# Optimization experiments

Measured on AMD Instinct MI355X. Metric: run time of the kernel, lower is better.

The kernel has to match this reference:

```python
import jax, jax.numpy as jnp
import numpy as np
from jax import lax

PRE_NMS_TOP_N = 2000
POST_NMS_TOP_N = 1000
NMS_THRESH = 0.7
MIN_SIZE = 0.0
BBOX_XFORM_CLIP = float(np.log(1000.0 / 16.0))
NEG = jnp.float32(-1e30)


def setup_inputs() -> dict:
    key = jax.random.key(0)
    k1, k2, k3, k4, k5 = jax.random.split(key, 5)
    N, A, H, W = 16, 3, 256, 336
    img_h, img_w = 1024, 1344
    num = A * H * W  # 258048 anchors per image
    objectness = jax.random.normal(k1, (N, A, H, W), jnp.float32)
    box_regression = jax.random.normal(k2, (N, A * 4, H, W), jnp.float32) * 0.5
    # synthetic but valid xyxy anchors (x2 > x1, y2 > y1)
    cx = jax.random.uniform(k3, (N, num)) * img_w
    cy = jax.random.uniform(k4, (N, num)) * img_h
    wh = 16.0 + jax.random.uniform(k5, (N, num, 2)) * 256.0
    anchors = jnp.stack([cx - 0.5 * wh[..., 0], cy - 0.5 * wh[..., 1],
                         cx + 0.5 * wh[..., 0], cy + 0.5 * wh[..., 1]], axis=-1)
    return {"anchors": anchors.astype(jnp.float32), "objectness": objectness,
            "box_regression": box_regression, "img_h": img_h, "img_w": img_w}


def box_decode(codes, anchors):
    # BoxCoder(weights=(1,1,1,1)).decode, TO_REMOVE=1 convention
    w = anchors[..., 2] - anchors[..., 0] + 1.0
    h = anchors[..., 3] - anchors[..., 1] + 1.0
    ctr_x = anchors[..., 0] + 0.5 * w
    ctr_y = anchors[..., 1] + 0.5 * h
    dx, dy, dw, dh = codes[..., 0], codes[..., 1], codes[..., 2], codes[..., 3]
    dw = jnp.minimum(dw, BBOX_XFORM_CLIP)
    dh = jnp.minimum(dh, BBOX_XFORM_CLIP)
    pcx = dx * w + ctr_x
    pcy = dy * h + ctr_y
    pw = jnp.exp(dw) * w
    ph = jnp.exp(dh) * h
    return jnp.stack([pcx - 0.5 * pw, pcy - 0.5 * ph,
                      pcx + 0.5 * pw - 1.0, pcy + 0.5 * ph - 1.0], axis=-1)


def pairwise_iou(boxes):
    area = (boxes[:, 2] - boxes[:, 0] + 1.0) * (boxes[:, 3] - boxes[:, 1] + 1.0)
    lt = jnp.maximum(boxes[:, None, :2], boxes[None, :, :2])  # [K,K,2]
    rb = jnp.minimum(boxes[:, None, 2:], boxes[None, :, 2:])
    wh = jnp.maximum(rb - lt + 1.0, 0.0)
    inter = wh[..., 0] * wh[..., 1]
    return inter / (area[:, None] + area[None, :] - inter)


def nms_keep(boxes, valid):
    # boxes already sorted by score desc; greedy suppression scan over rows
    K = boxes.shape[0]
    iou = pairwise_iou(boxes)  # [K,K]
    idx = jnp.arange(K)

    def body(keep, xs):
        row, i = xs
        sup = keep[i] & (idx > i) & (row > NMS_THRESH)
        return keep & ~sup, None

    keep, _ = lax.scan(body, valid, (iou, idx))
    return keep


def reference(anchors, objectness, box_regression, img_h, img_w):
    N, A, H, W = objectness.shape
    # permute_and_flatten: (N,A,H,W) -> (N, H*W*A)
    obj = jax.nn.sigmoid(jnp.transpose(objectness, (0, 2, 3, 1)).reshape(N, -1))
    breg = jnp.transpose(box_regression.reshape(N, A, 4, H, W), (0, 3, 4, 1, 2)).reshape(N, -1, 4)
    k = min(PRE_NMS_TOP_N, obj.shape[1])
    scores, topk_idx = lax.top_k(obj, k)  # sorted desc
    batch = jnp.arange(N)[:, None]
    breg = breg[batch, topk_idx]        # [N,k,4]
    anc = anchors[batch, topk_idx]      # [N,k,4]
    boxes = box_decode(breg, anc)       # [N,k,4]
    # clip_to_image (TO_REMOVE=1)
    x1 = jnp.clip(boxes[..., 0], 0.0, img_w - 1)
    y1 = jnp.clip(boxes[..., 1], 0.0, img_h - 1)
    x2 = jnp.clip(boxes[..., 2], 0.0, img_w - 1)
    y2 = jnp.clip(boxes[..., 3], 0.0, img_h - 1)
    boxes = jnp.stack([x1, y1, x2, y2], axis=-1)
    # remove_small_boxes as a validity mask (fixed shape)
    ws = x2 - x1 + 1.0
    hs = y2 - y1 + 1.0
    valid = (ws >= MIN_SIZE) & (hs >= MIN_SIZE)
    keep = jax.vmap(nms_keep)(boxes, valid)  # [N,k]
    masked = jnp.where(keep, scores, NEG)
    final_scores, sel = lax.top_k(masked, POST_NMS_TOP_N)  # preserves score order
    final_boxes = boxes[batch, sel]
    # [N, post_nms_top_n, 5]: xyxy + objectness (padded slots have score ~ -1e30)
    return jnp.concatenate([final_boxes, final_scores[..., None]], axis=-1)
```

## Files before the change

kernel.cpp:

```cpp
#include <hip/hip_runtime.h>
#include <stdint.h>

#define NIMG 16
#define AANCH 3
#define HH 256
#define WW 336
#define HWP (HH*WW)
#define NUM (AANCH*HWP)
#define TOTAL (NIMG*NUM)
#define PRE_K 2000
#define POST_K 1000
#define NMS_TH 0.7f
#define NEGV -1e30f
#define CAND_CAP 4096
#define ROWS 2048
#define RWORDS 64
#define CHUNK 4096
#define CBLOCKS (NUM / CHUNK)
#define HPARTS 16
#define HBINS 4096
#define HCHUNK (NUM / HPARTS)

#define WS_HIST 0u
#define WS_COLT 0u
#define WS_CBOX 262144u
#define WS_CSCO 1310720u
#define WS_CUT  4194304u
#define WS_CNT  4194560u
#define WS_CAND 4194816u
#define WS_BOX  4719104u
#define WS_SCO  5243392u
#define WS_RMI  5374464u
#define WS_MASK 5444096u

__device__ __forceinline__ uint32_t fkey(float f){
    uint32_t b = __float_as_uint(f);
    return (b & 0x80000000u) ? ~b : (b | 0x80000000u);
}
__device__ __forceinline__ float keyf(uint32_t k){
    uint32_t b = (k & 0x80000000u) ? (k & 0x7FFFFFFFu) : ~k;
    return __uint_as_float(b);
}

__global__ __launch_bounds__(1024) void k_hist(const float* __restrict__ obj,
                                               uint32_t* __restrict__ part,
                                               uint32_t* __restrict__ cnt,
                                               uint32_t* __restrict__ rminit){
    int img = blockIdx.x >> 4;
    int blk = blockIdx.x & 15;
    int tid = threadIdx.x;
    if (blockIdx.x == 0){
        for (int i = tid; i < 32 + NIMG * RWORDS; i += 1024){
            if (i < 32) cnt[i] = 0u;
            else        rminit[i - 32] = 0u;
        }
    }
    __shared__ uint32_t h[HBINS];
    #pragma unroll
    for (int i = 0; i < HBINS / 1024; ++i) h[tid + i * 1024] = 0u;
    __syncthreads();
    const float* base = obj + (size_t)img * NUM + (size_t)blk * HCHUNK;
    for (int e = tid * 4; e < HCHUNK; e += 4096){
        float4 v = *(const float4*)(base + e);
        atomicAdd(&h[fkey(v.x) >> 20], 1u);
        atomicAdd(&h[fkey(v.y) >> 20], 1u);
        atomicAdd(&h[fkey(v.z) >> 20], 1u);
        atomicAdd(&h[fkey(v.w) >> 20], 1u);
    }
    __syncthreads();
    uint32_t* p = part + ((size_t)blockIdx.x) * HBINS;
    #pragma unroll
    for (int i = 0; i < HBINS / 1024; ++i) p[tid + i * 1024] = h[tid + i * 1024];
}

__global__ __launch_bounds__(1024) void k_binsel(const uint32_t* __restrict__ part,
                                                 uint32_t* __restrict__ cut,
                                                 uint32_t* __restrict__ nAout){
    int img = blockIdx.x, tid = threadIdx.x;
    const uint32_t* pb = part + (size_t)img * HPARTS * HBINS;
    int bin0 = HBINS - 4 * (tid + 1);
    uint32_t c0 = 0, c1 = 0, c2 = 0, c3 = 0;
    for (int k = 0; k < HPARTS; ++k){
        const uint4 v = *(const uint4*)(pb + (size_t)k * HBINS + bin0);
        c0 += v.x; c1 += v.y; c2 += v.z; c3 += v.w;
    }
    uint32_t s = c0 + c1 + c2 + c3;
    __shared__ uint32_t ss[1024];
    uint32_t x = s;
    ss[tid] = x; __syncthreads();
    for (int d = 1; d < 1024; d <<= 1){
        uint32_t y = (tid >= d) ? ss[tid - d] : 0u;
        __syncthreads();
        x += y; ss[tid] = x;
        __syncthreads();
    }
    uint32_t incl = x, excl = x - s;
    if (excl < PRE_K && incl >= PRE_K){
        uint32_t c = excl;
        uint32_t cc[4] = {c0, c1, c2, c3};
        for (int j = 3; j >= 0; --j){
            uint32_t cb = c;
            c += cc[j];
            if (c >= PRE_K){
                cut[img] = ((uint32_t)(bin0 + j)) << 20;
                nAout[img] = cb;
                break;
            }
        }
    }
}

__device__ __forceinline__ void emit_candidate(
        uint32_t key, uint32_t f, uint32_t pos, int img,
        const float* __restrict__ anchors, const float* __restrict__ breg,
        float imw, float imh,
        unsigned long long* __restrict__ cand,
        float4* __restrict__ cboxes, float* __restrict__ cscores){
    const float CLIPV = 4.135166556742356f;
    cand[img * CAND_CAP + pos] = ((unsigned long long)key << 32)
        | ((unsigned long long)((~f) & 0x3FFFFu) << 14) | (unsigned long long)pos;
    float logit = keyf(key);
    float sc = 1.0f / (1.0f + expf(-logit));
    const float* an = anchors + ((size_t)img * NUM + f) * 4;
    float ax1 = an[0], ay1 = an[1], ax2 = an[2], ay2 = an[3];
    int a = (int)(f % AANCH); int hw = (int)(f / AANCH);
    size_t bbase = ((size_t)img * 12 + a * 4) * HWP + (size_t)hw;
    float dx = breg[bbase], dy = breg[bbase + HWP];
    float dw = breg[bbase + 2 * (size_t)HWP], dh = breg[bbase + 3 * (size_t)HWP];
    float aw = ax2 - ax1 + 1.0f, ah = ay2 - ay1 + 1.0f;
    float cx = ax1 + 0.5f * aw, cy = ay1 + 0.5f * ah;
    dw = fminf(dw, CLIPV); dh = fminf(dh, CLIPV);
    float pcx = dx * aw + cx, pcy = dy * ah + cy;
    float pw = expf(dw) * aw, ph = expf(dh) * ah;
    float x1 = pcx - 0.5f * pw, y1 = pcy - 0.5f * ph;
    float x2 = pcx + 0.5f * pw - 1.0f, y2 = pcy + 0.5f * ph - 1.0f;
    x1 = fminf(fmaxf(x1, 0.0f), imw - 1.0f);
    y1 = fminf(fmaxf(y1, 0.0f), imh - 1.0f);
    x2 = fminf(fmaxf(x2, 0.0f), imw - 1.0f);
    y2 = fminf(fmaxf(y2, 0.0f), imh - 1.0f);
    bool valid = ((x2 - x1 + 1.0f) >= 0.0f) && ((y2 - y1 + 1.0f) >= 0.0f);
    cboxes[img * CAND_CAP + pos] = make_float4(x1, y1, x2, y2);
    cscores[img * CAND_CAP + pos] = valid ? sc : -sc;
}

__global__ __launch_bounds__(256) void k_compact(const float* __restrict__ obj,
                                                 const uint32_t* __restrict__ cut,
                                                 const uint32_t* __restrict__ nAarr,
                                                 uint32_t* __restrict__ cnt,
                                                 unsigned long long* __restrict__ cand,
                                                 const float* __restrict__ anchors,
                                                 const float* __restrict__ breg,
                                                 const int* __restrict__ pimh,
                                                 const int* __restrict__ pimw,
                                                 float4* __restrict__ cboxes,
                                                 float* __restrict__ cscores){
    int img   = blockIdx.x / CBLOCKS;
    int chunk = blockIdx.x - img * CBLOCKS;
    int base  = img * NUM + chunk * CHUNK;
    __shared__ uint32_t lcA, lcB, gbA, gbB;
    __shared__ uint2 lbuf[CHUNK];
    if (threadIdx.x == 0){ lcA = 0u; lcB = 0u; }
    __syncthreads();
    uint32_t cutv = cut[img];
    uint32_t cutbin = cutv >> 20;
    float4 v[4];
    #pragma unroll
    for (int it = 0; it < 4; ++it)
        v[it] = *(const float4*)(obj + base + it * 1024 + (int)threadIdx.x * 4);
    #pragma unroll
    for (int it = 0; it < 4; ++it){
        int e = it * 1024 + (int)threadIdx.x * 4;
        float vv[4] = {v[it].x, v[it].y, v[it].z, v[it].w};
        #pragma unroll
        for (int q = 0; q < 4; ++q){
            uint32_t k = fkey(vv[q]);
            if (k >= cutv){
                int r = chunk * CHUNK + e + q;
                int a = r / HWP, hw = r - a * HWP;
                uint32_t f = (uint32_t)(hw * AANCH + a);
                if ((k >> 20) > cutbin){
                    uint32_t p = atomicAdd(&lcA, 1u);
                    lbuf[p] = make_uint2(k, f);
                } else {
                    uint32_t p = atomicAdd(&lcB, 1u);
                    lbuf[CHUNK - 1 - p] = make_uint2(k, f);
                }
            }
        }
    }
    __syncthreads();
    if (threadIdx.x == 0){
        gbA = (lcA > 0u) ? atomicAdd(&cnt[img], lcA) : 0u;
        gbB = (lcB > 0u) ? atomicAdd(&cnt[16 + img], lcB) : 0u;
    }
    __syncthreads();
    uint32_t nA  = nAarr[img];
    uint32_t nAp = (nA + 1u) & ~1u;
    float imw = (float)(*pimw), imh = (float)(*pimh);
    uint32_t na = lcA, ga = gbA, nb = lcB, gb = gbB;
    for (uint32_t t = threadIdx.x; t < na; t += 256u){
        uint32_t pos = ga + t;
        uint2 kf = lbuf[t];
        emit_candidate(kf.x, kf.y, pos, img, anchors, breg, imw, imh,
                       cand, cboxes, cscores);
    }
    for (uint32_t t = threadIdx.x; t < nb; t += 256u){
        uint32_t pos = nAp + gb + t;
        if (pos < CAND_CAP){
            uint2 kf = lbuf[CHUNK - 1 - t];
            emit_candidate(kf.x, kf.y, pos, img, anchors, breg, imw, imh,
                           cand, cboxes, cscores);
        }
    }
}

__global__ __launch_bounds__(256) void k_rank(
        const unsigned long long* __restrict__ cand, const uint32_t* __restrict__ cnt,
        const uint32_t* __restrict__ nAarr,
        const float4* __restrict__ cboxes, const float* __restrict__ cscores,
        float4* __restrict__ boxes_s, float* __restrict__ scores_s,
        uint32_t* __restrict__ rminit){
    int img = blockIdx.x >> 4;
    int b   = blockIdx.x & 15;
    int tid = threadIdx.x;
    int e   = b * 256 + tid;
    uint32_t nA   = nAarr[img];
    uint32_t nAp  = (nA + 1u) & ~1u;
    uint32_t nB   = min(cnt[16 + img], (uint32_t)CAND_CAP - nAp);
    uint32_t end  = nAp + nB;
    uint32_t endp = (end + 1u) & ~1u;
    const unsigned long long* cp = cand + img * CAND_CAP;
    __shared__ alignas(16) unsigned long long tile[CAND_CAP];
    for (int i = tid; i < (int)endp; i += 256){
        bool v = (i < (int)nA) || (i >= (int)nAp && i < (int)end);
        tile[i] = v ? cp[i] : 0ull;
    }
    __syncthreads();
    bool inA = e < (int)nA;
    bool inB = (e >= (int)nAp) && (e < (int)end);
    bool validE = inA || inB;
    unsigned long long mine = validE ? tile[e] : ~0ull;
    int s0 = inA ? 0 : (inB ? (int)(nAp >> 1) : 0);
    int s1 = inA ? (int)(nAp >> 1) : (inB ? (int)(endp >> 1) : 0);
    int rank = inB ? (int)nA : 0;
    const ulonglong2* tile2 = (const ulonglong2*)tile;
    #pragma unroll 8
    for (int i = s0; i < s1; ++i){
        ulonglong2 p = tile2[i];
        rank += (p.x > mine) ? 1 : 0;
        rank += (p.y > mine) ? 1 : 0;
    }
    if (validE && rank < PRE_K){
        float4 bx = cboxes[img * CAND_CAP + e];
        float s   = cscores[img * CAND_CAP + e];
        boxes_s[img * ROWS + rank] = bx;
        scores_s[img * ROWS + rank] = fabsf(s);
        if (s < 0.0f) atomicOr(&rminit[img * RWORDS + (rank >> 5)], 1u << (rank & 31));
    }
}

__global__ __launch_bounds__(1024) void k_mask(const float4* __restrict__ boxes_s,
                                               uint32_t* __restrict__ mask,
                                               unsigned long long* __restrict__ colT){
    int img = blockIdx.x >> 4;
    int rc  = blockIdx.x & 15;
    int tid = threadIdx.x;
    int lane = tid & 63;
    int wv = tid >> 6;
    int gw = rc * 16 + wv;
    __shared__ float4 B[ROWS];
    __shared__ float  AR[ROWS];
    const float4* bp = boxes_s + img * ROWS;
    for (int t = tid; t < ROWS; t += 1024){
        float4 b = bp[t]; B[t] = b;
        AR[t] = (b.z - b.x + 1.0f) * (b.w - b.y + 1.0f);
    }
    __syncthreads();
    if (gw < 32){
        int j = lane;
        float4 bj = B[gw * 64 + j]; float aj = AR[gw * 64 + j];
        unsigned long long col = 0ull;
        #pragma unroll 8
        for (int i = 0; i < 64; ++i){
            float4 bi = B[gw * 64 + i]; float ai = AR[gw * 64 + i];
            float xx1 = fmaxf(bi.x, bj.x), yy1 = fmaxf(bi.y, bj.y);
            float xx2 = fminf(bi.z, bj.z), yy2 = fminf(bi.w, bj.w);
            float iw = fmaxf(xx2 - xx1 + 1.0f, 0.0f);
            float ih = fmaxf(yy2 - yy1 + 1.0f, 0.0f);
            float inter = iw * ih;
            bool pred = (i < j) && (inter > NMS_TH * (ai + aj - inter));
            col |= pred ? (1ull << i) : 0ull;
        }
        colT[(size_t)(img * 32 + gw) * 64 + j] = col;
    }
    uint32_t* M = mask + (size_t)img * ROWS * RWORDS;
    for (int i = gw; i < PRE_K; i += 256){
        float4 bi = B[i];
        float ai = AR[i];
        unsigned long long* Mrow = (unsigned long long*)(M + (size_t)i * RWORDS);
        for (int jb = (i >> 6); jb < 32; ++jb){
            int j = (jb << 6) + lane;
            bool pred = false;
            if (j > i && j < PRE_K){
                float4 bj = B[j];
                float xx1 = fmaxf(bi.x, bj.x), yy1 = fmaxf(bi.y, bj.y);
                float xx2 = fminf(bi.z, bj.z), yy2 = fminf(bi.w, bj.w);
                float iw = fmaxf(xx2 - xx1 + 1.0f, 0.0f);
                float ih = fmaxf(yy2 - yy1 + 1.0f, 0.0f);
                float inter = iw * ih;
                pred = inter > NMS_TH * (ai + AR[j] - inter);
            }
            unsigned long long bm = __ballot(pred);
            if (lane == 0) Mrow[jb] = bm;
        }
    }
}

__global__ __launch_bounds__(256) void k_scan(const uint32_t* __restrict__ mask,
                                              const unsigned long long* __restrict__ colT,
                                              const uint32_t* __restrict__ rminit,
                                              const float4* __restrict__ boxes_s,
                                              const float* __restrict__ scores_s,
                                              float* __restrict__ out){
    int img = blockIdx.x;
    int tid = threadIdx.x;
    int lane = tid & 63;
    int wv = tid >> 6;
    const uint32_t* M = mask + (size_t)img * ROWS * RWORDS;
    const unsigned long long* CT = colT + (size_t)img * 32 * 64;
    __shared__ uint32_t S[POST_K];
    __shared__ uint32_t acc_lds[4][64];
    __shared__ unsigned long long keep_lds;

    uint32_t rm = 0u;
    if (wv == 0){
        rm = rminit[img * RWORDS + lane];
        if (lane == 62) rm |= 0xFFFF0000u;
        if (lane == 63) rm  = 0xFFFFFFFFu;
    }
    unsigned long long colA = 0ull, colB = 0ull, rmb_sav = 0ull;
    uint32_t rowsA[16], rowsB[16];

#define PRELOAD(B, ROWSX)                                                       \
    {                                                                           \
        const uint32_t* Mb = M + (size_t)((B) * 64 + wv * 16) * RWORDS + lane;  \
        _Pragma("unroll")                                                       \
        for (int r = 0; r < 16; ++r) ROWSX[r] = Mb[(size_t)r * RWORDS];         \
    }
#define FIXED_POINT(B, COLX)                                                    \
    {                                                                           \
        uint32_t lo = __shfl(rm, 2 * (B)), hi = __shfl(rm, 2 * (B) + 1);        \
        unsigned long long inc = ((unsigned long long)hi << 32)                 \
                               | (unsigned long long)lo;                        \
        bool alivej = ((inc >> lane) & 1ull) == 0ull;                           \
        unsigned long long keep = ~inc;                                         \
        for (int it = 0; it < 66; ++it){                                        \
            bool ok = alivej && ((COLX & keep) == 0ull);                        \
            unsigned long long nk = __ballot(ok);                              \
            if (nk == keep) break;                                              \
            keep = nk;                                                          \
        }                                                                       \
        if (lane == 0) keep_lds = keep;                                         \
        rmb_sav = ~keep;                                                        \
    }
#define APPLY(ROWSX)                                                            \
    {                                                                           \
        unsigned long long kp = keep_lds;                                       \
        uint32_t acc = 0u;                                                      \
        _Pragma("unroll")                                                       \
        for (int r = 0; r < 16; ++r)                                            \
            acc |= ((kp >> (wv * 16 + r)) & 1ull) ? ROWSX[r] : 0u;              \
        acc_lds[wv][lane] = acc;                                                \
    }
#define FINISH(B)                                                               \
    {                                                                           \
        uint32_t acc = acc_lds[0][lane] | acc_lds[1][lane]                      \
                     | acc_lds[2][lane] | acc_lds[3][lane];                     \
        rm |= (lane >= 2 * (B)) ? acc : 0u;                                     \
        if (lane == 2 * (B))     rm = (uint32_t)rmb_sav;                        \
        if (lane == 2 * (B) + 1) rm = (uint32_t)(rmb_sav >> 32);                \
    }

    PRELOAD(0, rowsA);
    if (wv == 0) colA = CT[lane];

    #pragma unroll 1
    for (int b = 0; b < 32; b += 2){
        PRELOAD(b + 1, rowsB);
        if (wv == 0){
            colB = CT[(size_t)(b + 1) * 64 + lane];
            FIXED_POINT(b, colA);
        }
        __syncthreads();
        APPLY(rowsA);
        __syncthreads();
        if (wv == 0) FINISH(b);
        if (b + 2 < 32){
            PRELOAD(b + 2, rowsA);
            if (wv == 0) colA = CT[(size_t)(b + 2) * 64 + lane];
        }
        if (wv == 0) FIXED_POINT(b + 1, colB);
        __syncthreads();
        APPLY(rowsB);
        __syncthreads();
        if (wv == 0) FINISH(b + 1);
    }
#undef PRELOAD
#undef FIXED_POINT
#undef APPLY
#undef FINISH

    if (wv == 0){
        uint32_t inr = (lane < 62) ? 0xFFFFFFFFu : (lane == 62 ? 0x0000FFFFu : 0u);
        uint32_t kw = (~rm) & inr;
        uint32_t sw = rm & inr;
        uint32_t kc = __popc(kw);
        uint32_t x = kc;
        for (int d = 1; d < 64; d <<= 1){ uint32_t y = __shfl_up(x, d); if (lane >= d) x += y; }
        uint32_t kexcl = x - kc;
        uint32_t ktot = __shfl(x, 63);
        uint32_t m = kw; uint32_t r = 0;
        while (m){
            int bb = __ffs(m) - 1;
            uint32_t slot = kexcl + r;
            if (slot < POST_K) S[slot] = (uint32_t)(lane * 32 + bb) | 0x80000000u;
            m &= m - 1; ++r;
        }
        if (ktot < POST_K){
            uint32_t sc2 = __popc(sw);
            uint32_t x2 = sc2;
            for (int d = 1; d < 64; d <<= 1){ uint32_t y = __shfl_up(x2, d); if (lane >= d) x2 += y; }
            uint32_t sexcl = x2 - sc2;
            uint32_t m2 = sw; uint32_t r2 = 0;
            while (m2){
                int bb = __ffs(m2) - 1;
                uint32_t slot = ktot + sexcl + r2;
                if (slot >= ktot && slot < POST_K) S[slot] = (uint32_t)(lane * 32 + bb);
                m2 &= m2 - 1; ++r2;
            }
        }
    }
    __syncthreads();
    const float4* bp = boxes_s + img * ROWS;
    const float* sp = scores_s + img * ROWS;
    float* o = out + (size_t)img * POST_K * 5;
    for (int s = tid; s < POST_K; s += 256){
        uint32_t v = S[s];
        uint32_t pos = v & 0x7FFFFFFFu;
        bool kept = (v >> 31) != 0;
        float4 bx = bp[pos];
        float sc = kept ? sp[pos] : NEGV;
        float* oo = o + s * 5;
        oo[0] = bx.x; oo[1] = bx.y; oo[2] = bx.z; oo[3] = bx.w; oo[4] = sc;
    }
}

extern "C" void kernel_launch(void* const* d_in, const int* in_sizes, int n_in,
                              void* d_out, int out_size, void* d_ws, size_t ws_size,
                              hipStream_t stream) {
    const float* anchors = (const float*)d_in[0];
    const float* obj     = (const float*)d_in[1];
    const float* breg    = (const float*)d_in[2];
    const int*   pimh    = (const int*)d_in[3];
    const int*   pimw    = (const int*)d_in[4];
    float* out = (float*)d_out;
    uint8_t* ws = (uint8_t*)d_ws;

    uint32_t*           part     = (uint32_t*)(ws + WS_HIST);
    unsigned long long* colT     = (unsigned long long*)(ws + WS_COLT);
    float4*             cboxes   = (float4*)(ws + WS_CBOX);
    float*              cscores  = (float*)(ws + WS_CSCO);
    uint32_t*           cut      = (uint32_t*)(ws + WS_CUT);
    uint32_t*           nAarr    = (uint32_t*)(ws + WS_CUT + 64);
    uint32_t*           cnt      = (uint32_t*)(ws + WS_CNT);
    unsigned long long* cand     = (unsigned long long*)(ws + WS_CAND);
    float4*             boxes_s  = (float4*)(ws + WS_BOX);
    float*              scores_s = (float*)(ws + WS_SCO);
    uint32_t*           rminit   = (uint32_t*)(ws + WS_RMI);
    uint32_t*           mask     = (uint32_t*)(ws + WS_MASK);

    k_hist<<<NIMG * HPARTS, 1024, 0, stream>>>(obj, part, cnt, rminit);
    k_binsel<<<NIMG, 1024, 0, stream>>>(part, cut, nAarr);
    k_compact<<<NIMG * CBLOCKS, 256, 0, stream>>>(obj, cut, nAarr, cnt, cand,
                                                  anchors, breg, pimh, pimw,
                                                  cboxes, cscores);
    k_rank<<<NIMG * 16, 256, 0, stream>>>(cand, cnt, nAarr, cboxes, cscores,
                                          boxes_s, scores_s, rminit);
    k_mask<<<NIMG * 16, 1024, 0, stream>>>(boxes_s, mask, colT);
    k_scan<<<NIMG, 256, 0, stream>>>(mask, colT, rminit, boxes_s, scores_s, out);
}
```

Before: 138.8 us.

## Restructure NMS mask kernel so each lane computes a whole row word

The IoU mask kernel now maps one row per lane: each lane owns box i and builds a 64-bit mask word per column block by looping over 64 broadcast column boxes from LDS. This replaces the previous per-row wave loop that used __ballot with a single lane storing. Each lane now writes a full 8-byte word, and LDS reads become broadcasts instead of per-lane gathers. Launch changes to 32 blocks of 512 threads per image, and areas are recomputed inline rather than cached in LDS. The trade-offs are more redundant area arithmetic and some load imbalance, since blocks for later row groups have fewer column blocks to process.

```diff
diff --git a/kernel.cpp b/kernel.cpp
--- a/kernel.cpp
+++ b/kernel.cpp
@@ -259,61 +259,82 @@
     }
 }
 
-__global__ __launch_bounds__(1024) void k_mask(const float4* __restrict__ boxes_s,
-                                               uint32_t* __restrict__ mask,
-                                               unsigned long long* __restrict__ colT){
-    int img = blockIdx.x >> 4;
-    int rc  = blockIdx.x & 15;
+__global__ __launch_bounds__(512) void k_mask(const float4* __restrict__ boxes_s,
+                                              uint32_t* __restrict__ mask,
+                                              unsigned long long* __restrict__ colT){
+    int img = blockIdx.x >> 5;
+    int ib  = blockIdx.x & 31;
     int tid = threadIdx.x;
     int lane = tid & 63;
     int wv = tid >> 6;
-    int gw = rc * 16 + wv;
     __shared__ float4 B[ROWS];
-    __shared__ float  AR[ROWS];
     const float4* bp = boxes_s + img * ROWS;
-    for (int t = tid; t < ROWS; t += 1024){
-        float4 b = bp[t]; B[t] = b;
-        AR[t] = (b.z - b.x + 1.0f) * (b.w - b.y + 1.0f);
-    }
-    __syncthreads();
-    if (gw < 32){
-        int j = lane;
-        float4 bj = B[gw * 64 + j]; float aj = AR[gw * 64 + j];
+    for (int t = tid; t < ROWS; t += 512) B[t] = bp[t];
+    __syncthreads();
+    int ik = (ib << 6) + lane;
+    float4 bi = B[ik];
+    float ai = (bi.z - bi.x + 1.0f) * (bi.w - bi.y + 1.0f);
+    uint32_t* M = mask + (size_t)img * ROWS * RWORDS;
+    unsigned long long* Mrow = (unsigned long long*)(M + (size_t)ik * RWORDS);
+
+#define IOU_BIT(BJ, EXTRA, WORD, BITM)                                          \
+    {                                                                           \
+        float aj = ((BJ).z-(BJ).x+1.0f)*((BJ).w-(BJ).y+1.0f);                   \
+        float xx1 = fmaxf(bi.x,(BJ).x), yy1 = fmaxf(bi.y,(BJ).y);               \
+        float xx2 = fminf(bi.z,(BJ).z), yy2 = fminf(bi.w,(BJ).w);               \
+        float iw = fmaxf(xx2-xx1+1.0f, 0.0f);                                   \
+        float ih = fmaxf(yy2-yy1+1.0f, 0.0f);                                   \
+        float inter = iw*ih;                                                    \
+        bool pred = (inter > NMS_TH*(ai+aj-inter)) && (EXTRA);                  \
+        WORD |= pred ? (BITM) : 0u;                                             \
+    }
+
+    if (wv == 0){
         unsigned long long col = 0ull;
         #pragma unroll 8
         for (int i = 0; i < 64; ++i){
-            float4 bi = B[gw * 64 + i]; float ai = AR[gw * 64 + i];
-            float xx1 = fmaxf(bi.x, bj.x), yy1 = fmaxf(bi.y, bj.y);
-            float xx2 = fminf(bi.z, bj.z), yy2 = fminf(bi.w, bj.w);
-            float iw = fmaxf(xx2 - xx1 + 1.0f, 0.0f);
-            float ih = fmaxf(yy2 - yy1 + 1.0f, 0.0f);
-            float inter = iw * ih;
-            bool pred = (i < j) && (inter > NMS_TH * (ai + aj - inter));
+            float4 bI = B[(ib << 6) + i];
+            float aI = (bI.z-bI.x+1.0f)*(bI.w-bI.y+1.0f);
+            float xx1 = fmaxf(bI.x, bi.x), yy1 = fmaxf(bI.y, bi.y);
+            float xx2 = fminf(bI.z, bi.z), yy2 = fminf(bI.w, bi.w);
+            float iw = fmaxf(xx2-xx1+1.0f, 0.0f);
+            float ih = fmaxf(yy2-yy1+1.0f, 0.0f);
+            float inter = iw*ih;
+            bool pred = (i < lane) && (inter > NMS_TH*(aI+ai-inter));
             col |= pred ? (1ull << i) : 0ull;
         }
-        colT[(size_t)(img * 32 + gw) * 64 + j] = col;
-    }
-    uint32_t* M = mask + (size_t)img * ROWS * RWORDS;
-    for (int i = gw; i < PRE_K; i += 256){
-        float4 bi = B[i];
-        float ai = AR[i];
-        unsigned long long* Mrow = (unsigned long long*)(M + (size_t)i * RWORDS);
-        for (int jb = (i >> 6); jb < 32; ++jb){
-            int j = (jb << 6) + lane;
-            bool pred = false;
-            if (j > i && j < PRE_K){
-                float4 bj = B[j];
-                float xx1 = fmaxf(bi.x, bj.x), yy1 = fmaxf(bi.y, bj.y);
-                float xx2 = fminf(bi.z, bj.z), yy2 = fminf(bi.w, bj.w);
-                float iw = fmaxf(xx2 - xx1 + 1.0f, 0.0f);
-                float ih = fmaxf(yy2 - yy1 + 1.0f, 0.0f);
-                float inter = iw * ih;
-                pred = inter > NMS_TH * (ai + AR[j] - inter);
-            }
-            unsigned long long bm = __ballot(pred);
-            if (lane == 0) Mrow[jb] = bm;
-        }
-    }
+        colT[(size_t)(img * 32 + ib) * 64 + lane] = col;
+        uint32_t lo = 0u, hi = 0u;
+        #pragma unroll
+        for (int j = 0; j < 32; ++j){
+            float4 bj = B[(ib << 6) + j];
+            IOU_BIT(bj, ((ib << 6) + j) > ik, lo, 1u << j);
+        }
+        #pragma unroll
+        for (int j = 0; j < 32; ++j){
+            float4 bj = B[(ib << 6) + 32 + j];
+            IOU_BIT(bj, ((ib << 6) + 32 + j) > ik, hi, 1u << j);
+        }
+        if (ib == 31){ hi = 0u; lo &= 0xFFFFu; }
+        Mrow[ib] = ((unsigned long long)hi << 32) | (unsigned long long)lo;
+    }
+    #pragma unroll 1
+    for (int jb = ib + 1 + wv; jb < 32; jb += 8){
+        uint32_t lo = 0u, hi = 0u;
+        #pragma unroll
+        for (int j = 0; j < 32; ++j){
+            float4 bj = B[(jb << 6) + j];
+            IOU_BIT(bj, true, lo, 1u << j);
+        }
+        #pragma unroll
+        for (int j = 0; j < 32; ++j){
+            float4 bj = B[(jb << 6) + 32 + j];
+            IOU_BIT(bj, true, hi, 1u << j);
+        }
+        if (jb == 31){ hi = 0u; lo &= 0xFFFFu; }
+        Mrow[jb] = ((unsigned long long)hi << 32) | (unsigned long long)lo;
+    }
+#undef IOU_BIT
 }
 
 __global__ __launch_bounds__(256) void k_scan(const uint32_t* __restrict__ mask,
@@ -486,6 +507,6 @@
                                                   cboxes, cscores);
     k_rank<<<NIMG * 16, 256, 0, stream>>>(cand, cnt, nAarr, cboxes, cscores,
                                           boxes_s, scores_s, rminit);
-    k_mask<<<NIMG * 16, 1024, 0, stream>>>(boxes_s, mask, colT);
+    k_mask<<<NIMG * 32, 512, 0, stream>>>(boxes_s, mask, colT);
     k_scan<<<NIMG, 256, 0, stream>>>(mask, colT, rminit, boxes_s, scores_s, out);
 }
```

Measured after the change: 143.5 us. +3.4%, slower.
